# Kernel tuning notes

Measured on AMD Instinct MI355X. Metric: run time of the kernel, lower is better.

Reference implementation:

```python
import jax, jax.numpy as jnp
import numpy as np

B, S, H = 2, 2048, 2048
N_HEADS = 16
HEAD_DIM = H // N_HEADS


def setup_inputs() -> dict:
    key = jax.random.key(0)
    ks = jax.random.split(key, 9)
    s = 1.0 / np.sqrt(H)
    inp = {
        "x": jax.random.normal(ks[0], (B, S, H), dtype=jnp.float32),
        "wq": jax.random.uniform(ks[1], (H, H), jnp.float32, -s, s),
        "bq": jnp.zeros((H,), jnp.float32),
        "wk": jax.random.uniform(ks[2], (H, H), jnp.float32, -s, s),
        "bk": jnp.zeros((H,), jnp.float32),
        "wv": jax.random.uniform(ks[3], (H, H), jnp.float32, -s, s),
        "bv": jnp.zeros((H,), jnp.float32),
        "wo": jax.random.uniform(ks[4], (H, H), jnp.float32, -s, s),
        "bo": jnp.zeros((H,), jnp.float32),
    }
    return inp


def reference(x, wq, bq, wk, bk, wv, bv, wo, bo):
    bsz, seq_len, hidden = x.shape
    scale = HEAD_DIM ** -0.5
    # projections -> [b, h, s, d]
    def proj(w, b):
        y = jnp.einsum("bsh,oh->bso", x, w) + b
        return y.reshape(bsz, seq_len, N_HEADS, HEAD_DIM).transpose(0, 2, 1, 3)
    q = proj(wq, bq)
    k = proj(wk, bk)
    v = proj(wv, bv)
    scores = jnp.einsum("bhqd,bhkd->bhqk", q, k) * scale
    causal = jnp.tril(jnp.ones((seq_len, seq_len), dtype=bool))
    scores = jnp.where(causal, scores, -jnp.inf)
    attn = jax.nn.softmax(scores, axis=-1)
    out = jnp.einsum("bhqk,bhkd->bhqd", attn, v)
    out = out.transpose(0, 2, 1, 3).reshape(bsz, seq_len, hidden)
    return jnp.einsum("bsh,oh->bso", out, wo) + bo
```

## Files before the change

### kernel.cpp

```cpp
#include <hip/hip_runtime.h>
#include <hip/hip_bf16.h>
#include <cstdint>
#include <cstddef>

#define BATCH 2
#define S_LEN 2048
#define HID   2048
#define NH    16
#define HD    128
#define GK    2048
#define NT    (GK / 64)
#define NIT   (NT / 2)
#define ATT_TILES (32 * NH * BATCH)

typedef short bf16x8 __attribute__((ext_vector_type(8)));
typedef float f32x4  __attribute__((ext_vector_type(4)));

__device__ inline unsigned short f2bf(float f) {
    unsigned int u = __float_as_uint(f);
    unsigned int r = (u + 0x7fffu + ((u >> 16) & 1u)) >> 16;
    return (unsigned short)r;
}

__global__ __launch_bounds__(256) void conv_f32_bf16(const float* __restrict__ src,
                                                     unsigned short* __restrict__ dst,
                                                     long n) {
    long i = ((long)blockIdx.x * 256 + threadIdx.x) * 8;
    if (i >= n) return;
    const float4 a = *(const float4*)(src + i);
    const float4 b = *(const float4*)(src + i + 4);
    union { unsigned short u[8]; bf16x8 v; } o;
    o.u[0] = f2bf(a.x); o.u[1] = f2bf(a.y); o.u[2] = f2bf(a.z); o.u[3] = f2bf(a.w);
    o.u[4] = f2bf(b.x); o.u[5] = f2bf(b.y); o.u[6] = f2bf(b.z); o.u[7] = f2bf(b.w);
    *(bf16x8*)(dst + i) = o.v;
}

__global__ __launch_bounds__(256) void conv4_f32_bf16(const float* __restrict__ s0,
                                                      const float* __restrict__ s1,
                                                      const float* __restrict__ s2,
                                                      const float* __restrict__ s3,
                                                      unsigned short* __restrict__ d0,
                                                      unsigned short* __restrict__ d1,
                                                      unsigned short* __restrict__ d2,
                                                      unsigned short* __restrict__ d3,
                                                      long n) {
    const int z = blockIdx.y;
    const float* src = (z == 0) ? s0 : (z == 1) ? s1 : (z == 2) ? s2 : s3;
    unsigned short* dst = (z == 0) ? d0 : (z == 1) ? d1 : (z == 2) ? d2 : d3;
    long i = ((long)blockIdx.x * 256 + threadIdx.x) * 8;
    if (i >= n) return;
    const float4 a = *(const float4*)(src + i);
    const float4 b = *(const float4*)(src + i + 4);
    union { unsigned short u[8]; bf16x8 v; } o;
    o.u[0] = f2bf(a.x); o.u[1] = f2bf(a.y); o.u[2] = f2bf(a.z); o.u[3] = f2bf(a.w);
    o.u[4] = f2bf(b.x); o.u[5] = f2bf(b.y); o.u[6] = f2bf(b.z); o.u[7] = f2bf(b.w);
    *(bf16x8*)(dst + i) = o.v;
}

__global__ void zero_int(int* p) { *p = 0; }


#define STAGE(DU, SRC, KT, H) do {                                            \
    const unsigned short* _s0 = (SRC) + (size_t)((H) * 128) * GK + (KT) * 64; \
    __builtin_amdgcn_global_load_lds(                                         \
        (const __attribute__((address_space(1))) void*)_s0,                   \
        (__attribute__((address_space(3))) void*)(Sm + (DU) + (H) * 8192 + sdst), \
        16, 0, 0);                                                            \
    __builtin_amdgcn_global_load_lds(                                         \
        (const __attribute__((address_space(1))) void*)(_s0 + (size_t)64 * GK), \
        (__attribute__((address_space(3))) void*)(Sm + (DU) + (H) * 8192 + 4096 + sdst), \
        16, 0, 0);                                                            \
} while (0)

#define READ_A(D, HI) do { _Pragma("unroll")                                  \
    for (int mi = 0; mi < 2; ++mi) {                                          \
        const int r_ = wm * 64 + ((HI) * 2 + mi) * 16 + ln;                   \
        a[(HI)*2+mi][0] = *(const bf16x8*)&Sm[(D) * 24576 + r_ * 64 + sw0];   \
        a[(HI)*2+mi][1] = *(const bf16x8*)&Sm[(D) * 24576 + r_ * 64 + sw1];   \
    } } while (0)

#define READ_B(D, HI) do { _Pragma("unroll")                                  \
    for (int ni = 0; ni < 2; ++ni) {                                          \
        const int r_ = wn * 64 + ((HI) * 2 + ni) * 16 + ln;                   \
        b[(HI)*2+ni][0] = *(const bf16x8*)&Sm[(D) * 24576 + 16384 + r_ * 64 + sw0]; \
        b[(HI)*2+ni][1] = *(const bf16x8*)&Sm[(D) * 24576 + 16384 + r_ * 64 + sw1]; \
    } } while (0)

#define MFMA8(MA, NA) do { _Pragma("unroll")                                  \
    for (int mi = 0; mi < 2; ++mi) _Pragma("unroll")                          \
    for (int ni = 0; ni < 2; ++ni) _Pragma("unroll")                          \
    for (int ks = 0; ks < 2; ++ks)                                            \
        acc[(MA)*2+mi][(NA)*2+ni] = __builtin_amdgcn_mfma_f32_16x16x32_bf16(  \
            a[(MA)*2+mi][ks], b[(NA)*2+ni][ks], acc[(MA)*2+mi][(NA)*2+ni], 0, 0, 0); \
} while (0)

#define PH_BEGIN  __builtin_amdgcn_s_barrier();                               \
                  asm volatile("s_waitcnt lgkmcnt(0)" ::: "memory");          \
                  __builtin_amdgcn_s_setprio(1)
#define PH_END    __builtin_amdgcn_s_setprio(0); __builtin_amdgcn_s_barrier()
#define PH_END_V2 __builtin_amdgcn_s_setprio(0);                              \
                  asm volatile("s_waitcnt vmcnt(2)" ::: "memory");            \
                  __builtin_amdgcn_s_barrier()
#define PH_END_V4 __builtin_amdgcn_s_setprio(0);                              \
                  asm volatile("s_waitcnt vmcnt(4)" ::: "memory");            \
                  __builtin_amdgcn_s_barrier()

__device__ __forceinline__ void gemm256_core(const unsigned short* __restrict__ A,
                                             const unsigned short* __restrict__ Bw,
                                             const float* __restrict__ bias,
                                             void* __restrict__ Cout,
                                             int mode, int M0, int N0,
                                             unsigned short* Sm) {
    const int tid  = threadIdx.x;
    const int lane = tid & 63;
    const int wave = tid >> 6;
    const int ln = lane & 15, g = lane >> 4;
    const int wm = wave & 3, wn = wave >> 2;

    const int strow = tid >> 3;
    const int stcol = (((tid & 7) ^ ((tid >> 3) & 7)) << 3);
    const unsigned short* gA = A  + (size_t)(M0 + strow) * GK + stcol;
    const unsigned short* gB = Bw + (size_t)(N0 + strow) * GK + stcol;
    const int sdst = wave * 512;

    const int sw0 = ((g    ) ^ (ln & 7)) << 3;
    const int sw1 = ((g + 4) ^ (ln & 7)) << 3;

    f32x4 acc[4][4];
#pragma unroll
    for (int i = 0; i < 4; ++i)
#pragma unroll
        for (int j = 0; j < 4; ++j) acc[i][j] = (f32x4){0.f, 0.f, 0.f, 0.f};
    bf16x8 a[4][2], b[4][2];

    STAGE(0,     gA, 0, 0); STAGE(0,     gA, 0, 1);
    STAGE(16384, gB, 0, 0);
    STAGE(24576, gA, 1, 0); STAGE(24576, gA, 1, 1);
    asm volatile("s_waitcnt vmcnt(4)" ::: "memory");
    __builtin_amdgcn_s_barrier();

    for (int it = 0; it < NIT; ++it) {
        const int kt1 = 2 * it + 1;
        const int kt2 = (2 * it + 2 < NT) ? 2 * it + 2 : NT - 1;
        const int kt3 = (2 * it + 3 < NT) ? 2 * it + 3 : NT - 1;
        READ_A(0, 0); READ_B(0, 0);
        STAGE(40960, gB, kt1, 0);
        PH_BEGIN; MFMA8(0, 0); PH_END;
        READ_B(0, 1);
        PH_BEGIN; MFMA8(0, 1); PH_END;
        READ_A(0, 1);
        STAGE(16384, gB, kt2, 0);
        PH_BEGIN; MFMA8(1, 0); PH_END;
        PH_BEGIN; MFMA8(1, 1); PH_END_V2;
        READ_A(1, 0); READ_B(1, 0);
        STAGE(0, gA, kt2, 0);
        PH_BEGIN; MFMA8(0, 0); PH_END;
        READ_B(1, 1);
        STAGE(0, gA, kt2, 1);
        PH_BEGIN; MFMA8(0, 1); PH_END;
        READ_A(1, 1);
        PH_BEGIN; MFMA8(1, 0); PH_END;
        STAGE(24576, gA, kt3, 0); STAGE(24576, gA, kt3, 1);
        PH_BEGIN; MFMA8(1, 1); PH_END_V4;
    }
    asm volatile("s_waitcnt vmcnt(0)" ::: "memory");
    __syncthreads();

    if (mode == 0) {
        const int bb = M0 >> 11;
        const int sb = M0 & (S_LEN - 1);
        const int h  = N0 >> 7;
#pragma unroll
        for (int nf = 0; nf < 4; ++nf) {
            const int d = wn * 64 + nf * 16 + ln;
            const float bn = bias[N0 + d];
            unsigned short* dst = (unsigned short*)Cout +
                (((size_t)(bb * NH + h) * S_LEN + sb + wm * 64) * HD + d);
#pragma unroll
            for (int mf = 0; mf < 4; ++mf)
#pragma unroll
                for (int r = 0; r < 4; ++r)
                    dst[(size_t)(mf * 16 + g * 4 + r) * HD] = f2bf(acc[mf][nf][r] + bn);
        }
    } else if (mode == 2) {
        float* dst = (float*)Cout;
#pragma unroll
        for (int nf = 0; nf < 4; ++nf) {
            const int n = N0 + wn * 64 + nf * 16 + ln;
            const float bn = bias[n];
#pragma unroll
            for (int mf = 0; mf < 4; ++mf)
#pragma unroll
                for (int r = 0; r < 4; ++r) {
                    const int m = M0 + wm * 64 + mf * 16 + g * 4 + r;
                    dst[(size_t)m * HID + n] = acc[mf][nf][r] + bn;
                }
        }
    } else {
        const int bb = M0 >> 11;
        const int sb = M0 & (S_LEN - 1);
        const int h  = N0 >> 7;
#pragma unroll
        for (int p = 0; p < 2; ++p) {
            if ((wm >> 1) == p) {
#pragma unroll
                for (int nf = 0; nf < 4; ++nf) {
                    const int dl = wn * 64 + nf * 16 + ln;
                    const float bn = bias[N0 + dl];
#pragma unroll
                    for (int mf = 0; mf < 4; ++mf) {
                        const int sl = (wm & 1) * 64 + mf * 16 + g * 4;
                        const int cs = (sl >> 3) ^ (dl & 15);
                        union { unsigned short u[4]; unsigned long long q; } pk;
#pragma unroll
                        for (int r = 0; r < 4; ++r) pk.u[r] = f2bf(acc[mf][nf][r] + bn);
                        *(unsigned long long*)&Sm[dl * 128 + cs * 8 + (sl & 7)] = pk.q;
                    }
                }
            }
            __syncthreads();
            {
                const int dl = tid >> 2;
                unsigned short* dst = (unsigned short*)Cout +
                    ((size_t)(bb * NH + h) * HD + dl) * S_LEN + sb + p * 128;
#pragma unroll
                for (int jj = 0; jj < 4; ++jj) {
                    const int sc = (tid & 3) + jj * 4;
                    const int cs = sc ^ (dl & 15);
                    *(bf16x8*)(dst + sc * 8) = *(const bf16x8*)&Sm[dl * 128 + cs * 8];
                }
            }
            __syncthreads();
        }
    }
}

__global__ __launch_bounds__(512, 2) void gemm_qkv256(
        const unsigned short* __restrict__ A,
        const unsigned short* __restrict__ w0, const unsigned short* __restrict__ w1,
        const unsigned short* __restrict__ w2,
        const float* __restrict__ b0, const float* __restrict__ b1,
        const float* __restrict__ b2,
        void* o0, void* o1, void* o2) {
    extern __shared__ __align__(16) unsigned short Sm[];
    const int z = blockIdx.z;
    const unsigned short* Bw = (z == 0) ? w0 : (z == 1) ? w1 : w2;
    const float* bias = (z == 0) ? b0 : (z == 1) ? b1 : b2;
    void* Cout = (z == 0) ? o0 : (z == 1) ? o1 : o2;
    gemm256_core(A, Bw, bias, Cout, (z == 2) ? 1 : 0,
                 blockIdx.y * 256, blockIdx.x * 128, Sm);
}

__global__ __launch_bounds__(512, 2) void gemm_out256(
        const unsigned short* __restrict__ A, const unsigned short* __restrict__ Bw,
        const float* __restrict__ bias, float* __restrict__ Cout) {
    extern __shared__ __align__(16) unsigned short Sm[];
    gemm256_core(A, Bw, bias, Cout, 2, blockIdx.y * 256, blockIdx.x * 128, Sm);
}

__global__ __launch_bounds__(256) void attn_kernel(const unsigned short* __restrict__ Q,
                                                   const unsigned short* __restrict__ Kk,
                                                   const unsigned short* __restrict__ Vt,
                                                   unsigned short* __restrict__ O,
                                                   int* __restrict__ ticket) {
    __shared__ __align__(16) unsigned short Ks[64 * 128];
    __shared__ __align__(16) unsigned short Vs[144 * 64];
    __shared__ __align__(16) unsigned short Pl[4][16 * 72];
    __shared__ int tsh;
    const int tid = threadIdx.x;
    const int lane = tid & 63;
    const int wave = tid >> 6;
    const int g = lane >> 4, ln = lane & 15;
    const float scale2 = 0.08838834764831845f * 1.4426950408889634f;

    for (int i = tid; i < 16 * 64; i += 256) Vs[128 * 64 + i] = 0x3F80;

    const int kcol = ((tid & 15) ^ ((tid >> 4) & 15)) * 8;
    const int vcol = ((tid & 7) ^ ((tid >> 3) & 7)) * 8;

    for (;;) {
        if (tid == 0) tsh = atomicAdd(ticket, 1);
        __syncthreads();
        const int t = tsh;
        if (t >= ATT_TILES) break;
        const int qt = 31 - (t >> 5);
        const int bh = t & 31;
        const int qbase = qt * 64 + wave * 16;

        const unsigned short* Qp = Q  + (size_t)bh * S_LEN * HD;
        const unsigned short* Kp = Kk + (size_t)bh * S_LEN * HD;
        const unsigned short* Vp = Vt + (size_t)bh * HD * S_LEN;

        bf16x8 aq[4];
#pragma unroll
        for (int dc = 0; dc < 4; ++dc)
            aq[dc] = *(const bf16x8*)&Qp[(size_t)(qbase + ln) * HD + dc * 32 + g * 8];

        f32x4 acc[9];
#pragma unroll
        for (int i = 0; i < 9; ++i) acc[i] = (f32x4){0.f, 0.f, 0.f, 0.f};

        for (int kt = 0; kt <= qt; ++kt) {
            const int kb = kt * 64;
#pragma unroll
            for (int i = 0; i < 4; ++i) {
                const unsigned short* gk = Kp + (size_t)(kb + i * 16 + (tid >> 4)) * HD + kcol;
                __builtin_amdgcn_global_load_lds(
                    (const __attribute__((address_space(1))) void*)gk,
                    (__attribute__((address_space(3))) void*)(Ks + i * 2048 + wave * 512),
                    16, 0, 0);
            }
#pragma unroll
            for (int i = 0; i < 4; ++i) {
                const unsigned short* gv = Vp + (size_t)(i * 32 + (tid >> 3)) * S_LEN + kb + vcol;
                __builtin_amdgcn_global_load_lds(
                    (const __attribute__((address_space(1))) void*)gv,
                    (__attribute__((address_space(3))) void*)(Vs + i * 2048 + wave * 512),
                    16, 0, 0);
            }
            __syncthreads();
            f32x4 sc[4];
#pragma unroll
            for (int nc = 0; nc < 4; ++nc) {
                sc[nc] = (f32x4){0.f, 0.f, 0.f, 0.f};
#pragma unroll
                for (int dc = 0; dc < 4; ++dc) {
                    bf16x8 bk = *(const bf16x8*)&Ks[(nc * 16 + ln) * 128 + ((dc * 4 + g) ^ ln) * 8];
                    sc[nc] = __builtin_amdgcn_mfma_f32_16x16x32_bf16(aq[dc], bk, sc[nc], 0, 0, 0);
                }
            }
            const bool diag = (kt == qt);
#pragma unroll
            for (int nc = 0; nc < 4; ++nc)
#pragma unroll
                for (int r = 0; r < 4; ++r) {
                    float pv = __builtin_amdgcn_exp2f(sc[nc][r] * scale2);
                    if (diag && (nc * 16 + ln > wave * 16 + g * 4 + r)) pv = 0.f;
                    Pl[wave][(g * 4 + r) * 72 + nc * 16 + ln] = f2bf(pv);
                }
#pragma unroll
            for (int kc = 0; kc < 2; ++kc) {
                bf16x8 ap = *(const bf16x8*)&Pl[wave][ln * 72 + kc * 32 + g * 8];
#pragma unroll
                for (int d2 = 0; d2 < 9; ++d2) {
                    bf16x8 bv = *(const bf16x8*)&Vs[(d2 * 16 + ln) * 64 + ((kc * 4 + g) ^ (ln & 7)) * 8];
                    acc[d2] = __builtin_amdgcn_mfma_f32_16x16x32_bf16(ap, bv, acc[d2], 0, 0, 0);
                }
            }
            __syncthreads();
        }
        const int b = bh >> 4, h = bh & 15;
        float inv[4];
#pragma unroll
        for (int r = 0; r < 4; ++r) inv[r] = 1.0f / acc[8][r];
#pragma unroll
        for (int d2 = 0; d2 < 8; ++d2)
#pragma unroll
            for (int r = 0; r < 4; ++r) {
                const int row = qbase + g * 4 + r;
                const int col = h * HD + d2 * 16 + ln;
                O[((size_t)b * S_LEN + row) * HID + col] = f2bf(acc[d2][r] * inv[r]);
            }
    }
}

extern "C" void kernel_launch(void* const* d_in, const int* in_sizes, int n_in,
                              void* d_out, int out_size, void* d_ws, size_t ws_size,
                              hipStream_t stream) {
    const float* x  = (const float*)d_in[0];
    const float* wq = (const float*)d_in[1];
    const float* bq = (const float*)d_in[2];
    const float* wk = (const float*)d_in[3];
    const float* bk = (const float*)d_in[4];
    const float* wv = (const float*)d_in[5];
    const float* bv = (const float*)d_in[6];
    const float* wo = (const float*)d_in[7];
    const float* bo = (const float*)d_in[8];
    float* out = (float*)d_out;

    const long nx = (long)BATCH * S_LEN * HID;
    const long nw = (long)HID * HID;

    char* p = (char*)d_ws;
    unsigned short* xb  = (unsigned short*)p; p += nx * 2;
    unsigned short* wqb = (unsigned short*)p; p += nw * 2;
    unsigned short* wkb = (unsigned short*)p; p += nw * 2;
    unsigned short* wvb = (unsigned short*)p; p += nw * 2;
    unsigned short* wob = (unsigned short*)p; p += nw * 2;
    unsigned short* Qb  = (unsigned short*)p; p += nx * 2;
    unsigned short* Kb  = (unsigned short*)p; p += nx * 2;
    unsigned short* Vtb = (unsigned short*)p; p += nx * 2;
    unsigned short* Ob  = (unsigned short*)p; p += nx * 2;
    int* ticket = (int*)p;

    conv_f32_bf16<<<(int)(nx / 8 / 256), 256, 0, stream>>>(x, xb, nx);
    dim3 cgrid((unsigned)(nw / 8 / 256), 4);
    conv4_f32_bf16<<<cgrid, 256, 0, stream>>>(wq, wk, wv, wo, wqb, wkb, wvb, wob, nw);
    zero_int<<<1, 1, 0, stream>>>(ticket);

    const int M = BATCH * S_LEN;
    dim3 qkvgrid(HID / 128, M / 256, 3);
    gemm_qkv256<<<qkvgrid, 512, 98304, stream>>>(xb, wqb, wkb, wvb, bq, bk, bv,
                                                 Qb, Kb, Vtb);

    attn_kernel<<<768, 256, 0, stream>>>(Qb, Kb, Vtb, Ob, ticket);

    dim3 ogrid(HID / 128, M / 256);
    gemm_out256<<<ogrid, 512, 98304, stream>>>(Ob, wob, bo, out);
}
```

Baseline: 374.5 us.

## Double-buffer attention K/V loads, remap GEMM tiles per XCD, tune attention grid

The attention kernel now double-buffers K and V tiles in LDS, prefetching the next tile with async global-to-LDS loads while the current one is computed, using partial vmcnt waits and raw barriers. The row-sum is computed by an MFMA against a register constant of ones instead of a padded ones block in LDS, and the MFMA sections run at raised wave priority. Both GEMM kernels remap block indices so neighbouring tiles land on the same XCD, aiming for better L2 reuse. The persistent attention grid drops from 768 to 512 blocks with a two-block occupancy bound, trading resident waves for the larger LDS footprint.

Result: no change. 371.7 us (-0.8%).

```diff
diff --git a/kernel.cpp b/kernel.cpp
--- a/kernel.cpp
+++ b/kernel.cpp
@@ -235,6 +235,15 @@
     }
 }
 
+__device__ __forceinline__ void xcd_remap(int& M0, int& N0) {
+    const int f = blockIdx.y * gridDim.x + blockIdx.x;
+    const int c = f & 7, j = f >> 3;
+    const int nx_ = 2 * c + (j & 1);
+    const int ny_ = j >> 1;
+    M0 = ny_ * 256;
+    N0 = nx_ * 128;
+}
+
 __global__ __launch_bounds__(512, 2) void gemm_qkv256(
         const unsigned short* __restrict__ A,
         const unsigned short* __restrict__ w0, const unsigned short* __restrict__ w1,
@@ -247,24 +256,25 @@
     const unsigned short* Bw = (z == 0) ? w0 : (z == 1) ? w1 : w2;
     const float* bias = (z == 0) ? b0 : (z == 1) ? b1 : b2;
     void* Cout = (z == 0) ? o0 : (z == 1) ? o1 : o2;
-    gemm256_core(A, Bw, bias, Cout, (z == 2) ? 1 : 0,
-                 blockIdx.y * 256, blockIdx.x * 128, Sm);
+    int M0, N0; xcd_remap(M0, N0);
+    gemm256_core(A, Bw, bias, Cout, (z == 2) ? 1 : 0, M0, N0, Sm);
 }
 
 __global__ __launch_bounds__(512, 2) void gemm_out256(
         const unsigned short* __restrict__ A, const unsigned short* __restrict__ Bw,
         const float* __restrict__ bias, float* __restrict__ Cout) {
     extern __shared__ __align__(16) unsigned short Sm[];
-    gemm256_core(A, Bw, bias, Cout, 2, blockIdx.y * 256, blockIdx.x * 128, Sm);
-}
-
-__global__ __launch_bounds__(256) void attn_kernel(const unsigned short* __restrict__ Q,
-                                                   const unsigned short* __restrict__ Kk,
-                                                   const unsigned short* __restrict__ Vt,
-                                                   unsigned short* __restrict__ O,
-                                                   int* __restrict__ ticket) {
-    __shared__ __align__(16) unsigned short Ks[64 * 128];
-    __shared__ __align__(16) unsigned short Vs[144 * 64];
+    int M0, N0; xcd_remap(M0, N0);
+    gemm256_core(A, Bw, bias, Cout, 2, M0, N0, Sm);
+}
+
+__global__ __launch_bounds__(256, 2) void attn_kernel(const unsigned short* __restrict__ Q,
+                                                      const unsigned short* __restrict__ Kk,
+                                                      const unsigned short* __restrict__ Vt,
+                                                      unsigned short* __restrict__ O,
+                                                      int* __restrict__ ticket) {
+    __shared__ __align__(16) unsigned short Ks[2 * 64 * 128];
+    __shared__ __align__(16) unsigned short Vs[2 * 128 * 64];
     __shared__ __align__(16) unsigned short Pl[4][16 * 72];
     __shared__ int tsh;
     const int tid = threadIdx.x;
@@ -272,8 +282,7 @@
     const int wave = tid >> 6;
     const int g = lane >> 4, ln = lane & 15;
     const float scale2 = 0.08838834764831845f * 1.4426950408889634f;
-
-    for (int i = tid; i < 16 * 64; i += 256) Vs[128 * 64 + i] = 0x3F80;
+    const bf16x8 ones_v = {0x3F80, 0x3F80, 0x3F80, 0x3F80, 0x3F80, 0x3F80, 0x3F80, 0x3F80};
 
     const int kcol = ((tid & 15) ^ ((tid >> 4) & 15)) * 8;
     const int vcol = ((tid & 7) ^ ((tid >> 3) & 7)) * 8;
@@ -300,35 +309,68 @@
 #pragma unroll
         for (int i = 0; i < 9; ++i) acc[i] = (f32x4){0.f, 0.f, 0.f, 0.f};
 
+#pragma unroll
+        for (int i = 0; i < 4; ++i) {
+            const unsigned short* gk = Kp + (size_t)(i * 16 + (tid >> 4)) * HD + kcol;
+            __builtin_amdgcn_global_load_lds(
+                (const __attribute__((address_space(1))) void*)gk,
+                (__attribute__((address_space(3))) void*)(Ks + i * 2048 + wave * 512),
+                16, 0, 0);
+        }
+#pragma unroll
+        for (int i = 0; i < 4; ++i) {
+            const unsigned short* gv = Vp + (size_t)(i * 32 + (tid >> 3)) * S_LEN + vcol;
+            __builtin_amdgcn_global_load_lds(
+                (const __attribute__((address_space(1))) void*)gv,
+                (__attribute__((address_space(3))) void*)(Vs + i * 2048 + wave * 512),
+                16, 0, 0);
+        }
+
         for (int kt = 0; kt <= qt; ++kt) {
-            const int kb = kt * 64;
-#pragma unroll
-            for (int i = 0; i < 4; ++i) {
-                const unsigned short* gk = Kp + (size_t)(kb + i * 16 + (tid >> 4)) * HD + kcol;
-                __builtin_amdgcn_global_load_lds(
-                    (const __attribute__((address_space(1))) void*)gk,
-                    (__attribute__((address_space(3))) void*)(Ks + i * 2048 + wave * 512),
-                    16, 0, 0);
-            }
-#pragma unroll
-            for (int i = 0; i < 4; ++i) {
-                const unsigned short* gv = Vp + (size_t)(i * 32 + (tid >> 3)) * S_LEN + kb + vcol;
-                __builtin_amdgcn_global_load_lds(
-                    (const __attribute__((address_space(1))) void*)gv,
-                    (__attribute__((address_space(3))) void*)(Vs + i * 2048 + wave * 512),
-                    16, 0, 0);
-            }
-            __syncthreads();
+            const int cur = kt & 1;
+            const bool do_stage = (kt + 1 <= qt);
+            if (do_stage) {
+                const int kb2 = (kt + 1) * 64;
+                const int nb  = (kt + 1) & 1;
+                unsigned short* kdst = Ks + nb * 8192 + wave * 512;
+                unsigned short* vdst = Vs + nb * 8192 + wave * 512;
+#pragma unroll
+                for (int i = 0; i < 4; ++i) {
+                    const unsigned short* gk = Kp + (size_t)(kb2 + i * 16 + (tid >> 4)) * HD + kcol;
+                    __builtin_amdgcn_global_load_lds(
+                        (const __attribute__((address_space(1))) void*)gk,
+                        (__attribute__((address_space(3))) void*)(kdst + i * 2048),
+                        16, 0, 0);
+                }
+#pragma unroll
+                for (int i = 0; i < 4; ++i) {
+                    const unsigned short* gv = Vp + (size_t)(i * 32 + (tid >> 3)) * S_LEN + kb2 + vcol;
+                    __builtin_amdgcn_global_load_lds(
+                        (const __attribute__((address_space(1))) void*)gv,
+                        (__attribute__((address_space(3))) void*)(vdst + i * 2048),
+                        16, 0, 0);
+                }
+            }
+            if (kt == 0 || !do_stage) {
+                asm volatile("s_waitcnt vmcnt(0)" ::: "memory");
+            } else {
+                asm volatile("s_waitcnt vmcnt(8)" ::: "memory");
+            }
+            __builtin_amdgcn_s_barrier();
+
+            const int kbuf = cur * 8192;
             f32x4 sc[4];
+            __builtin_amdgcn_s_setprio(1);
 #pragma unroll
             for (int nc = 0; nc < 4; ++nc) {
                 sc[nc] = (f32x4){0.f, 0.f, 0.f, 0.f};
 #pragma unroll
                 for (int dc = 0; dc < 4; ++dc) {
-                    bf16x8 bk = *(const bf16x8*)&Ks[(nc * 16 + ln) * 128 + ((dc * 4 + g) ^ ln) * 8];
+                    bf16x8 bk = *(const bf16x8*)&Ks[kbuf + (nc * 16 + ln) * 128 + ((dc * 4 + g) ^ ln) * 8];
                     sc[nc] = __builtin_amdgcn_mfma_f32_16x16x32_bf16(aq[dc], bk, sc[nc], 0, 0, 0);
                 }
             }
+            __builtin_amdgcn_s_setprio(0);
             const bool diag = (kt == qt);
 #pragma unroll
             for (int nc = 0; nc < 4; ++nc)
@@ -338,16 +380,19 @@
                     if (diag && (nc * 16 + ln > wave * 16 + g * 4 + r)) pv = 0.f;
                     Pl[wave][(g * 4 + r) * 72 + nc * 16 + ln] = f2bf(pv);
                 }
+            __builtin_amdgcn_s_setprio(1);
 #pragma unroll
             for (int kc = 0; kc < 2; ++kc) {
                 bf16x8 ap = *(const bf16x8*)&Pl[wave][ln * 72 + kc * 32 + g * 8];
 #pragma unroll
-                for (int d2 = 0; d2 < 9; ++d2) {
-                    bf16x8 bv = *(const bf16x8*)&Vs[(d2 * 16 + ln) * 64 + ((kc * 4 + g) ^ (ln & 7)) * 8];
+                for (int d2 = 0; d2 < 8; ++d2) {
+                    bf16x8 bv = *(const bf16x8*)&Vs[kbuf + (d2 * 16 + ln) * 64 + ((kc * 4 + g) ^ (ln & 7)) * 8];
                     acc[d2] = __builtin_amdgcn_mfma_f32_16x16x32_bf16(ap, bv, acc[d2], 0, 0, 0);
                 }
-            }
-            __syncthreads();
+                acc[8] = __builtin_amdgcn_mfma_f32_16x16x32_bf16(ap, ones_v, acc[8], 0, 0, 0);
+            }
+            __builtin_amdgcn_s_setprio(0);
+            __builtin_amdgcn_s_barrier();
         }
         const int b = bh >> 4, h = bh & 15;
         float inv[4];
@@ -403,7 +448,7 @@
     gemm_qkv256<<<qkvgrid, 512, 98304, stream>>>(xb, wqb, wkb, wvb, bq, bk, bv,
                                                  Qb, Kb, Vtb);
 
-    attn_kernel<<<768, 256, 0, stream>>>(Qb, Kb, Vtb, Ob, ticket);
+    attn_kernel<<<512, 256, 0, stream>>>(Qb, Kb, Vtb, Ob, ticket);
 
     dim3 ogrid(HID / 128, M / 256);
     gemm_out256<<<ogrid, 512, 98304, stream>>>(Ob, wob, bo, out);
```
